# Performance work log

Measured on AMD Instinct MI355X. Metric: run time of the kernel, lower is better.

The kernel has to match this reference:

```python
import jax, jax.numpy as jnp
import numpy as np

V, C, D = 25, 64, 64          # joints, in_channels, out_channels
N, T = 64, 300                # batch, frames
WEIGHT = 2
GROUPS = [[0, 12], [13, 24]]
BN_EPS = 1e-5


def _inner_shift(A, graph_group, node, channels, weight):
    """Faithful numpy port of Modified_grouped_shift_gcn.inner_shift."""
    index_array = np.arange(node * channels).reshape(node, channels)
    copy = index_array.copy()
    for grp in graph_group:
        lb, ub = int(np.min(grp)), int(np.max(grp)) + 1
        for i in range(lb, ub):
            cur = A[i].copy()
            cur[i] = 0
            neighbors = np.nonzero(cur)[0]
            j = 0
            ci = i - lb + 1
            while j < channels:
                nxt = ci % (ub - lb) + lb
                if j < weight:
                    j += weight
                elif nxt == i:
                    j += weight
                    ci += 1
                elif nxt in neighbors:
                    index_array[i][j:j + weight] = copy[nxt][j:j + weight]
                    j += weight
                    ci += 1
                else:
                    index_array[i][j] = copy[nxt][j]
                    j += 1
                    ci += 1
    return index_array.flatten()


def _adjacency():
    # chain skeleton with self loops, binarized as in __init__
    A = np.zeros((V, V), dtype=np.float64)
    for i in range(V - 1):
        A[i, i + 1] = 1.0
        A[i + 1, i] = 1.0
    np.fill_diagonal(A, 1.0)
    return A


def setup_inputs() -> dict:
    key = jax.random.key(0)
    k0, k1, k2, k3 = jax.random.split(key, 4)
    A = _adjacency()
    shift_in = jnp.asarray(_inner_shift(A, GROUPS, V, C, WEIGHT), dtype=jnp.int32)
    shift_out = jnp.asarray(_inner_shift(A, GROUPS, V, D, WEIGHT), dtype=jnp.int32)
    x0 = jax.random.normal(k0, (N, C, T, V), dtype=jnp.float32)
    feature_mask = 0.1 * jax.random.normal(k1, (1, V, C), dtype=jnp.float32)
    W = jax.random.normal(k2, (C, D), dtype=jnp.float32) * np.float32(np.sqrt(1.0 / D))
    b = 0.01 * jax.random.normal(k3, (1, 1, D), dtype=jnp.float32)
    gamma = jnp.ones((V * D,), dtype=jnp.float32)
    beta = jnp.zeros((V * D,), dtype=jnp.float32)
    return {"x0": x0, "feature_mask": feature_mask, "W": W, "b": b,
            "gamma": gamma, "beta": beta,
            "shift_in": shift_in, "shift_out": shift_out}


def reference(x0, feature_mask, W, b, gamma, beta, shift_in, shift_out):
    n, c, t, v = x0.shape
    # (n, c, t, v) -> (n*t, v*c)
    x = jnp.transpose(x0, (0, 2, 3, 1)).reshape(n * t, v * c)
    # channel-wise shift gather (precomputed permutation)
    x = x[:, shift_in].reshape(n * t, v, c)
    # learned feature mask
    x = x * (jnp.tanh(feature_mask) + 1.0)
    # pointwise linear + bias
    x = jnp.einsum('nvc,cd->nvd', x, W) + b
    x = x.reshape(n * t, v * W.shape[1])
    # second shift gather
    x = x[:, shift_out]
    # BatchNorm1d, training mode (biased batch stats)
    mean = jnp.mean(x, axis=0)
    var = jnp.var(x, axis=0)
    x = (x - mean) * jax.lax.rsqrt(var + BN_EPS) * gamma + beta
    # back to (n, d, t, v), residual (in==out so down is identity), relu
    x = x.reshape(n, t, v, W.shape[1]).transpose(0, 3, 1, 2)
    return jax.nn.relu(x + x0)
```

## Files before the change

### kernel.cpp

```cpp
#include <hip/hip_runtime.h>
#include <math.h>

#define V_ 25
#define C_ 64
#define D_ 64
#define N_ 64
#define T_ 300
#define R_ (N_*T_)
#define K_ (V_*C_)
#define BN_EPS 1e-5f

#define WS_GM     0
#define WS_SCALE  1600
#define WS_SHIFT  3200
#define WS_VP     4800
#define WS_SUM    6400
#define WS_SQ     8000
#define WS_WBF    9600

using bf16x8 = __attribute__((ext_vector_type(8))) short;
using f32x4  = __attribute__((ext_vector_type(4))) float;

__device__ __forceinline__ unsigned short f2bf(float f) {
    unsigned u = __float_as_uint(f);
    return (unsigned short)((u + 0x7FFFu + ((u >> 16) & 1u)) >> 16);
}

__global__ __launch_bounds__(256) void prep_tables(
    const float* __restrict__ fm, const float* __restrict__ W,
    const int* __restrict__ s_in, float* __restrict__ ws)
{
    int idx = blockIdx.x * 256 + threadIdx.x;
    if (idx < K_) {
        int jj  = s_in[idx];
        int off = (jj & 63) * 100 + (jj >> 6);
        unsigned mk = (unsigned)f2bf(tanhf(fm[idx]) + 1.0f);
        ((unsigned*)ws)[WS_GM + idx] = (mk << 16) | (unsigned)off;
    }
    if (idx < C_ * D_) ((unsigned short*)(ws + WS_WBF))[idx] = f2bf(W[idx]);
}

__global__ __launch_bounds__(256) void prep_scale_kernel(
    const float* __restrict__ gamma, const float* __restrict__ beta,
    const int* __restrict__ s_out, float* __restrict__ ws)
{
    int kk = blockIdx.x * 256 + threadIdx.x;
    if (kk < K_) {
        int dd = kk / 25;
        int v  = kk - dd * 25;
        int k  = v * 64 + dd;
        int jj = s_out[k];
        float mean = ws[WS_SUM + jj] * (1.0f / (float)R_);
        float var  = fmaf(-mean, mean, ws[WS_SQ + jj] * (1.0f / (float)R_));
        float inv  = rsqrtf(var + BN_EPS);
        float sc   = gamma[k] * inv;
        ws[WS_SCALE + kk] = sc;
        ws[WS_SHIFT + kk] = beta[k] - mean * sc;
        ((int*)ws)[WS_VP + kk] = jj;
    }
}

__device__ __forceinline__ void stage_xs(
    const float* __restrict__ xwin, float4* xs4, int tid)
{
    const float4* s4 = (const float4*)xwin;
    #pragma unroll
    for (int i = 0; i < 7; ++i) {
        int idx = i * 256 + tid;
        if (idx < 1600) {
            int c = idx / 25;
            int r = idx - c * 25;
            xs4[c * 25 + r] = s4[c * 1875 + r];
        }
    }
}

__device__ __forceinline__ void load_gmr(
    const unsigned* __restrict__ gmt, unsigned gmr[28], int lane, int w)
{
    int jw = lane & 3;
    int vh = lane >> 4;
    #pragma unroll
    for (int i = 0; i < 14; ++i) {
        int combo = i * 4 + w;
        int T  = combo >> 2;
        int q2 = combo & 3;
        int t  = T >> 1;
        int c0 = (T & 1) * 32 + q2 * 8 + jw * 2;
        int v  = t * 4 + vh;
        int kb = (v < V_) ? (v * 64 + c0) : c0;
        gmr[2 * i]     = gmt[kb];
        gmr[2 * i + 1] = gmt[kb + 1];
    }
}

__device__ __forceinline__ void build_afm(
    const float* xs, unsigned* a_fm32, const unsigned gmr[28], int lane, int w)
{
    int m  = lane >> 2;
    int jw = lane & 3;
    int dt = m & 3;
    #pragma unroll
    for (int i = 0; i < 14; ++i) {
        int combo = i * 4 + w;
        int T  = combo >> 2;
        int q2 = combo & 3;
        unsigned g0 = gmr[2 * i], g1 = gmr[2 * i + 1];
        float m0 = __uint_as_float(g0 & 0xFFFF0000u);
        float m1 = __uint_as_float(g1 & 0xFFFF0000u);
        float f0 = xs[(g0 & 0xFFFFu) + dt * 25] * m0;
        float f1 = xs[(g1 & 0xFFFFu) + dt * 25] * m1;
        a_fm32[(T * 64 + q2 * 16 + m) * 4 + jw] =
            (unsigned)f2bf(f0) | ((unsigned)f2bf(f1) << 16);
    }
}

__global__ __launch_bounds__(256, 4) void pass1_stats(
    const float* __restrict__ x0, const float* __restrict__ bg,
    float* __restrict__ ws)
{
    __shared__ __align__(16) float4 xs4[1600];
    __shared__ __align__(16) unsigned a_fm32[3584];
    const float* xs = (const float*)xs4;
    const bf16x8* afp = (const bf16x8*)a_fm32;

    int tid = threadIdx.x;
    int lane = tid & 63, w = tid >> 6;
    int l15 = lane & 15, q = lane >> 4;
    int d = w * 16 + l15;

    const unsigned short* Wbf = (const unsigned short*)(ws + WS_WBF);
    bf16x8 bfrag0, bfrag1;
    #pragma unroll
    for (int j = 0; j < 8; ++j) {
        bfrag0[j] = (short)Wbf[(q * 8 + j) * 64 + d];
        bfrag1[j] = (short)Wbf[(32 + q * 8 + j) * 64 + d];
    }
    float breg = bg[d];

    unsigned gmr[28];
    load_gmr((const unsigned*)ws + WS_GM, gmr, lane, w);

    float sums[7], sqs[7];
    #pragma unroll
    for (int t = 0; t < 7; ++t) { sums[t] = 0.f; sqs[t] = 0.f; }

    #pragma unroll 1
    for (int st = 0; st < 4; ++st) {
        int r0 = blockIdx.x * 16 + st * 4;
        int n  = r0 / 300;
        int t0 = r0 - n * 300;
        const float* xwin = x0 + (size_t)n * 480000 + t0 * 25;

        stage_xs(xwin, xs4, tid);
        __syncthreads();
        build_afm(xs, a_fm32, gmr, lane, w);
        __syncthreads();

        #pragma unroll
        for (int t = 0; t < 7; ++t) {
            bf16x8 a0 = afp[(t * 2 + 0) * 64 + lane];
            bf16x8 a1 = afp[(t * 2 + 1) * 64 + lane];
            f32x4 acc = {0.f, 0.f, 0.f, 0.f};
            acc = __builtin_amdgcn_mfma_f32_16x16x32_bf16(a0, bfrag0, acc, 0, 0, 0);
            acc = __builtin_amdgcn_mfma_f32_16x16x32_bf16(a1, bfrag1, acc, 0, 0, 0);
            #pragma unroll
            for (int r = 0; r < 4; ++r) {
                float y = acc[r] + breg;
                sums[t] += y;
                sqs[t]   = fmaf(y, y, sqs[t]);
            }
        }
        __syncthreads();
    }

    #pragma unroll
    for (int t = 0; t < 7; ++t) {
        int v = t * 4 + q;
        if (v < V_) {
            atomicAdd(&ws[WS_SUM + v * 64 + d], sums[t]);
            atomicAdd(&ws[WS_SQ  + v * 64 + d], sqs[t]);
        }
    }
}

__global__ __launch_bounds__(256, 4) void pass2_out(
    const float* __restrict__ x0, const float* __restrict__ bg,
    const float* __restrict__ ws, float* __restrict__ out)
{
    __shared__ __align__(16) char smem[25600 + 14336];
    float4* xs4   = (float4*)smem;
    const float* xs = (const float*)smem;
    float* y_lds  = (float*)smem;
    unsigned* a_fm32 = (unsigned*)(smem + 25600);
    const bf16x8* afp = (const bf16x8*)a_fm32;

    int tid = threadIdx.x;
    int lane = tid & 63, w = tid >> 6;
    int l15 = lane & 15, q = lane >> 4;
    int d = w * 16 + l15;

    const unsigned short* Wbf = (const unsigned short*)(ws + WS_WBF);
    bf16x8 bfrag0, bfrag1;
    #pragma unroll
    for (int j = 0; j < 8; ++j) {
        bfrag0[j] = (short)Wbf[(q * 8 + j) * 64 + d];
        bfrag1[j] = (short)Wbf[(32 + q * 8 + j) * 64 + d];
    }
    float breg = bg[d];

    unsigned gmr[28];
    load_gmr((const unsigned*)ws + WS_GM, gmr, lane, w);

    int r0 = blockIdx.x * 4;
    int n  = r0 / 300;
    int t0 = r0 - n * 300;
    const float* xwin = x0 + (size_t)n * 480000 + t0 * 25;

    stage_xs(xwin, xs4, tid);
    __syncthreads();
    build_afm(xs, a_fm32, gmr, lane, w);
    __syncthreads();

    #pragma unroll
    for (int t = 0; t < 7; ++t) {
        bf16x8 a0 = afp[(t * 2 + 0) * 64 + lane];
        bf16x8 a1 = afp[(t * 2 + 1) * 64 + lane];
        f32x4 acc = {0.f, 0.f, 0.f, 0.f};
        acc = __builtin_amdgcn_mfma_f32_16x16x32_bf16(a0, bfrag0, acc, 0, 0, 0);
        acc = __builtin_amdgcn_mfma_f32_16x16x32_bf16(a1, bfrag1, acc, 0, 0, 0);
        int v = t * 4 + q;
        if (v < V_) {
            #pragma unroll
            for (int r = 0; r < 4; ++r)
                y_lds[d * 100 + r * 25 + v] = acc[r] + breg;
        }
    }
    __syncthreads();

    const float* scp = ws + WS_SCALE;
    const float* shp = ws + WS_SHIFT;
    const int*   vpp = (const int*)ws + WS_VP;
    #pragma unroll
    for (int i = 0; i < 25; ++i) {
        int e   = i * 256 + tid;
        int dd  = e / 100;
        int rem = e - dd * 100;
        int dt  = rem / 25;
        int v   = rem - dt * 25;
        int kk  = dd * 25 + v;
        int jj  = vpp[kk];
        float z = y_lds[(jj & 63) * 100 + dt * 25 + (jj >> 6)];
        int ga  = (n * 64 + dd) * 7500 + (t0 + dt) * 25 + v;
        float val = fmaf(z, scp[kk], shp[kk]) + x0[ga];
        __builtin_nontemporal_store(fmaxf(val, 0.f), &out[ga]);
    }
}

extern "C" void kernel_launch(void* const* d_in, const int* in_sizes, int n_in,
                              void* d_out, int out_size, void* d_ws, size_t ws_size,
                              hipStream_t stream)
{
    const float* x0    = (const float*)d_in[0];
    const float* fm    = (const float*)d_in[1];
    const float* W     = (const float*)d_in[2];
    const float* b     = (const float*)d_in[3];
    const float* gamma = (const float*)d_in[4];
    const float* beta  = (const float*)d_in[5];
    const int*   s_in  = (const int*)d_in[6];
    const int*   s_out = (const int*)d_in[7];
    float* out = (float*)d_out;
    float* ws  = (float*)d_ws;

    (void)hipMemsetAsync(ws + WS_SUM, 0, 2 * K_ * sizeof(float), stream);
    prep_tables<<<16, 256, 0, stream>>>(fm, W, s_in, ws);
    pass1_stats<<<R_ / 16, 256, 0, stream>>>(x0, b, ws);
    prep_scale_kernel<<<7, 256, 0, stream>>>(gamma, beta, s_out, ws);
    pass2_out<<<R_ / 4, 256, 0, stream>>>(x0, b, ws, out);
}
```

Baseline: 313.6 us.

## Replace stats atomics with per-block partials, prefetch next window, double grid

Pass1 now runs twice as many blocks, each covering 8 rows instead of 16, and prefetches the next x window into registers while the current MFMA tile is computed. Instead of atomically adding into global sums, each block writes its partial sums and squares to a scratch buffer, which reuses the output tensor. A new stats_reduce kernel then sums those partials deterministically, and the memset is dropped. This removes atomic contention and hides load latency, at the cost of an extra kernel launch, about 30 MB of partial traffic, and more register pressure.

Result: slower. 363.8 us (+16.0%).

```diff
diff --git a/kernel.cpp b/kernel.cpp
--- a/kernel.cpp
+++ b/kernel.cpp
@@ -18,6 +18,8 @@
 #define WS_SQ     8000
 #define WS_WBF    9600
 
+#define P1_BLOCKS 2400
+
 using bf16x8 = __attribute__((ext_vector_type(8))) short;
 using f32x4  = __attribute__((ext_vector_type(4))) float;
 
@@ -38,6 +40,29 @@
         ((unsigned*)ws)[WS_GM + idx] = (mk << 16) | (unsigned)off;
     }
     if (idx < C_ * D_) ((unsigned short*)(ws + WS_WBF))[idx] = f2bf(W[idx]);
+}
+
+__global__ __launch_bounds__(256) void stats_reduce(
+    const float* __restrict__ pbuf, float* __restrict__ ws)
+{
+    __shared__ float red[256];
+    int jq = threadIdx.x & 15;
+    int bq = threadIdx.x >> 4;
+    int j  = blockIdx.x * 16 + jq;
+    const float* p = pbuf + (size_t)(bq * 150) * 3200 + j;
+    float s = 0.f;
+    #pragma unroll 10
+    for (int k = 0; k < 150; ++k)
+        s += p[(size_t)k * 3200];
+    red[threadIdx.x] = s;
+    __syncthreads();
+    if (bq < 8) red[threadIdx.x] += red[threadIdx.x + 128];
+    __syncthreads();
+    if (bq < 4) red[threadIdx.x] += red[threadIdx.x + 64];
+    __syncthreads();
+    if (bq < 2) red[threadIdx.x] += red[threadIdx.x + 32];
+    __syncthreads();
+    if (bq == 0) ws[WS_SUM + j] = red[jq] + red[jq + 16];
 }
 
 __global__ __launch_bounds__(256) void prep_scale_kernel(
@@ -75,6 +100,34 @@
     }
 }
 
+__device__ __forceinline__ void load_window_regs(
+    const float* __restrict__ xwin, float4 pf[7], int tid)
+{
+    const float4* s4 = (const float4*)xwin;
+    #pragma unroll
+    for (int i = 0; i < 7; ++i) {
+        int idx = i * 256 + tid;
+        if (idx < 1600) {
+            int c = idx / 25;
+            int r = idx - c * 25;
+            pf[i] = s4[c * 1875 + r];
+        }
+    }
+}
+__device__ __forceinline__ void store_window_regs(
+    const float4 pf[7], float4* xs4, int tid)
+{
+    #pragma unroll
+    for (int i = 0; i < 7; ++i) {
+        int idx = i * 256 + tid;
+        if (idx < 1600) {
+            int c = idx / 25;
+            int r = idx - c * 25;
+            xs4[c * 25 + r] = pf[i];
+        }
+    }
+}
+
 __device__ __forceinline__ void load_gmr(
     const unsigned* __restrict__ gmt, unsigned gmr[28], int lane, int w)
 {
@@ -117,7 +170,7 @@
 
 __global__ __launch_bounds__(256, 4) void pass1_stats(
     const float* __restrict__ x0, const float* __restrict__ bg,
-    float* __restrict__ ws)
+    const float* __restrict__ ws, float* __restrict__ pbuf)
 {
     __shared__ __align__(16) float4 xs4[1600];
     __shared__ __align__(16) unsigned a_fm32[3584];
@@ -145,15 +198,25 @@
     #pragma unroll
     for (int t = 0; t < 7; ++t) { sums[t] = 0.f; sqs[t] = 0.f; }
 
-    #pragma unroll 1
-    for (int st = 0; st < 4; ++st) {
-        int r0 = blockIdx.x * 16 + st * 4;
+    int r0base = blockIdx.x * 8;
+    float4 pf[7];
+    {
+        int r0 = r0base;
         int n  = r0 / 300;
         int t0 = r0 - n * 300;
-        const float* xwin = x0 + (size_t)n * 480000 + t0 * 25;
-
-        stage_xs(xwin, xs4, tid);
-        __syncthreads();
+        load_window_regs(x0 + (size_t)n * 480000 + t0 * 25, pf, tid);
+        store_window_regs(pf, xs4, tid);
+    }
+    __syncthreads();
+
+    #pragma unroll 1
+    for (int st = 0; st < 2; ++st) {
+        if (st < 1) {
+            int r0 = r0base + 4;
+            int n  = r0 / 300;
+            int t0 = r0 - n * 300;
+            load_window_regs(x0 + (size_t)n * 480000 + t0 * 25, pf, tid);
+        }
         build_afm(xs, a_fm32, gmr, lane, w);
         __syncthreads();
 
@@ -171,15 +234,18 @@
                 sqs[t]   = fmaf(y, y, sqs[t]);
             }
         }
+
+        if (st < 1) store_window_regs(pf, xs4, tid);
         __syncthreads();
     }
 
+    float* pout = pbuf + (size_t)blockIdx.x * 3200;
     #pragma unroll
     for (int t = 0; t < 7; ++t) {
         int v = t * 4 + q;
         if (v < V_) {
-            atomicAdd(&ws[WS_SUM + v * 64 + d], sums[t]);
-            atomicAdd(&ws[WS_SQ  + v * 64 + d], sqs[t]);
+            pout[v * 64 + d]        = sums[t];
+            pout[1600 + v * 64 + d] = sqs[t];
         }
     }
 }
@@ -272,9 +338,9 @@
     float* out = (float*)d_out;
     float* ws  = (float*)d_ws;
 
-    (void)hipMemsetAsync(ws + WS_SUM, 0, 2 * K_ * sizeof(float), stream);
     prep_tables<<<16, 256, 0, stream>>>(fm, W, s_in, ws);
-    pass1_stats<<<R_ / 16, 256, 0, stream>>>(x0, b, ws);
+    pass1_stats<<<P1_BLOCKS, 256, 0, stream>>>(x0, b, ws, out);
+    stats_reduce<<<200, 256, 0, stream>>>(out, ws);
     prep_scale_kernel<<<7, 256, 0, stream>>>(gamma, beta, s_out, ws);
     pass2_out<<<R_ / 4, 256, 0, stream>>>(x0, b, ws, out);
 }
```
